# Kernel tuning notes

Hardware: AMD Instinct MI355X
Metric: run time of the kernel (lower is better)

Reference implementation:

```python
import jax, jax.numpy as jnp
import numpy as np

B, S, D, H = 4, 1024, 1024, 16
HD = D // H  # head_dim = 64


def setup_inputs() -> dict:
    key = jax.random.key(0)
    ks = jax.random.split(key, 16)
    w = lambda k: jax.random.normal(k, (D, D), dtype=jnp.float32) * 0.02
    b = lambda k: jax.random.normal(k, (D,), dtype=jnp.float32) * 0.02
    x = jax.random.normal(ks[0], (B, S, D), dtype=jnp.float32)
    mask = jnp.tril(jnp.ones((S, S), dtype=jnp.int32))[None, None]  # causal [1,1,S,S]
    bar_indices = jax.random.randint(ks[1], (S,), 0, S, dtype=jnp.int64)
    beat_indices = jax.random.randint(ks[2], (S,), 0, S, dtype=jnp.int64)
    return {
        "x": x, "mask": mask, "bar_indices": bar_indices, "beat_indices": beat_indices,
        "Wq": w(ks[3]), "bq": b(ks[4]), "Wk": w(ks[5]), "bk": b(ks[6]),
        "Wv": w(ks[7]), "bv": b(ks[8]),
        "W_bark": w(ks[9]), "b_bark": b(ks[10]),
        "W_beatk": w(ks[11]), "b_beatk": b(ks[12]),
        "Wo": w(ks[13]), "bo": b(ks[14]),
    }


def reference(x, mask, bar_indices, beat_indices, Wq, bq, Wk, bk, Wv, bv,
              W_bark, b_bark, W_beatk, b_beatk, Wo, bo):
    Bs, Sl, Dm = x.shape
    heads, hd = H, Dm // H

    def proj(t, W, b):  # torch Linear: t @ W.T + b, then split heads -> [B,H,S,hd]
        y = t @ W.T + b
        return y.reshape(Bs, -1, heads, hd).transpose(0, 2, 1, 3)

    q = proj(x, Wq, bq)
    k = proj(x, Wk, bk)
    v = proj(x, Wv, bv)
    scale = 1.0 / jnp.sqrt(jnp.asarray(hd, x.dtype))

    scores = jnp.einsum('bhqd,bhkd->bhqk', q, k) * scale

    # hierarchical bar bias (bar_query is computed but unused in the original)
    bar_k = proj(x[:, bar_indices], W_bark, b_bark)
    scores = scores + 0.2 * (jnp.einsum('bhqd,bhkd->bhqk', q, bar_k) * scale)

    # hierarchical beat bias
    beat_k = proj(x[:, beat_indices], W_beatk, b_beatk)
    scores = scores + 0.1 * (jnp.einsum('bhqd,bhkd->bhqk', q, beat_k) * scale)

    scores = jnp.where(mask == 0, jnp.asarray(-1e9, scores.dtype), scores)
    attn = jax.nn.softmax(scores, axis=-1)  # dropout is identity in eval

    out = jnp.einsum('bhqk,bhkd->bhqd', attn, v)
    out = out.transpose(0, 2, 1, 3).reshape(Bs, Sl, Dm)
    return out @ Wo.T + bo
```

## Files before the change

kernel.cpp:

```cpp
#include <hip/hip_runtime.h>
#include <hip/hip_bf16.h>


typedef __bf16 bf16x8 __attribute__((ext_vector_type(8)));
typedef __bf16 bf16x4 __attribute__((ext_vector_type(4)));
typedef float  f32x4  __attribute__((ext_vector_type(4)));

#define DMODEL 1024

#define ASYNC_LOAD16(gp, lp)                                                  \
    __builtin_amdgcn_global_load_lds(                                         \
        (const __attribute__((address_space(1))) unsigned int*)(gp),          \
        (__attribute__((address_space(3))) unsigned int*)(lp), 16, 0, 0)

__global__ __launch_bounds__(256) void cvt_kernel(
    const float* __restrict__ x,
    const float* __restrict__ Wq, const float* __restrict__ Wk,
    const float* __restrict__ Wv, const float* __restrict__ Wbar,
    const float* __restrict__ Wbeat, const float* __restrict__ Wo,
    __bf16* __restrict__ dst)
{
    const int g = blockIdx.x * 256 + threadIdx.x;
    const size_t e = (size_t)g * 8;
    const int seg = (int)(e >> 20);
    const float* src; size_t off; float s = 1.0f;
    if (seg < 4)       { src = x;     off = e; }
    else if (seg == 4) { src = Wq;    off = e - ((size_t)4 << 20); }
    else if (seg == 5) { src = Wk;    off = e - ((size_t)5 << 20); }
    else if (seg == 6) { src = Wv;    off = e - ((size_t)6 << 20); }
    else if (seg == 7) { src = Wbar;  off = e - ((size_t)7 << 20); s = 0.2f; }
    else if (seg == 8) { src = Wbeat; off = e - ((size_t)8 << 20); s = 0.1f; }
    else               { src = Wo;    off = e - ((size_t)9 << 20); }
    const float4 a = *(const float4*)&src[off];
    const float4 b = *(const float4*)&src[off + 4];
    bf16x8 v;
    v[0] = (__bf16)(a.x * s); v[1] = (__bf16)(a.y * s);
    v[2] = (__bf16)(a.z * s); v[3] = (__bf16)(a.w * s);
    v[4] = (__bf16)(b.x * s); v[5] = (__bf16)(b.y * s);
    v[6] = (__bf16)(b.z * s); v[7] = (__bf16)(b.w * s);
    *(bf16x8*)&dst[e] = v;
}


#define SWZ_COL(r_, ks_) \
    (((((ks_) * 64) + quad * 16) ^ (((r_) & 7) << 4)) >> 1)

#define READ_ALL(c_)                                                          \
    do {                                                                      \
        _Pragma("unroll") for (int mh = 0; mh < 2; ++mh)                      \
        _Pragma("unroll") for (int mi = 0; mi < 2; ++mi) {                    \
            const int r_ = ((w >> 2) << 5) + mh * 64 + mi * 16 + l15;         \
            _Pragma("unroll") for (int ks = 0; ks < 2; ++ks)                  \
                af[mh][mi][ks] = *(const bf16x8*)&Alds[(c_) * 8192 +          \
                                        r_ * 64 + SWZ_COL(r_, ks)];           \
        }                                                                     \
        _Pragma("unroll") for (int nh = 0; nh < 2; ++nh)                      \
        _Pragma("unroll") for (int nj = 0; nj < 2; ++nj) {                    \
            const int r_ = ((w & 3) << 5) + nh * 128 + nj * 16 + l15;         \
            _Pragma("unroll") for (int ks = 0; ks < 2; ++ks)                  \
                bfr[nh][nj][ks] = *(const bf16x8*)&Blds[(c_) * 16384 +        \
                                        r_ * 64 + SWZ_COL(r_, ks)];           \
        }                                                                     \
    } while (0)

#define STAGE_A1(bufn_, h_, kt_)                                              \
    do {                                                                      \
        const int tm_ = (kt_) >> 4;                                           \
        const int k0_ = ((kt_) & 15) << 6;                                    \
        const __bf16* ap_ = (tm_ == 0) ? aA0##h_ : (tm_ == 1) ? aA1##h_       \
                                                              : aA2##h_;      \
        ASYNC_LOAD16(ap_ + k0_,                                               \
                     &Alds[(bufn_) * 8192 + (h_) * 4096 + w * 512]);          \
    } while (0)

#define STAGE_B2(bufn_, h_, kt_)                                              \
    do {                                                                      \
        const int tm_ = (kt_) >> 4;                                           \
        const int k0_ = ((kt_) & 15) << 6;                                    \
        const __bf16* wp_ = (tm_ == 0) ? W0 : (tm_ == 1) ? W1 : W2;           \
        ASYNC_LOAD16(wp_ + bro##h_##0 + k0_,                                  \
                     &Blds[(bufn_) * 16384 + (h_) * 8192 + w * 512]);         \
        ASYNC_LOAD16(wp_ + bro##h_##1 + k0_,                                  \
                     &Blds[(bufn_) * 16384 + (h_) * 8192 + 4096 + w * 512]);  \
    } while (0)

#define PHASE_BAR1()                                                          \
    do {                                                                      \
        __builtin_amdgcn_s_barrier();                                         \
        asm volatile("s_waitcnt lgkmcnt(0)" ::: "memory");                    \
    } while (0)

#define MFMA16(nh_)                                                           \
    do {                                                                      \
        __builtin_amdgcn_s_setprio(1);                                        \
        _Pragma("unroll") for (int mh = 0; mh < 2; ++mh)                      \
        _Pragma("unroll") for (int mi = 0; mi < 2; ++mi)                      \
        _Pragma("unroll") for (int nj = 0; nj < 2; ++nj)                      \
        _Pragma("unroll") for (int ks = 0; ks < 2; ++ks) {                    \
            acc[mh * 2 + mi][(nh_) * 2 + nj] =                                \
                __builtin_amdgcn_mfma_f32_16x16x32_bf16(                      \
                    af[mh][mi][ks], bfr[(nh_)][nj][ks],                       \
                    acc[mh * 2 + mi][(nh_) * 2 + nj], 0, 0, 0);               \
        }                                                                     \
        __builtin_amdgcn_s_setprio(0);                                        \
    } while (0)

__global__ __launch_bounds__(512, 2) void gemm8p_kernel(
    const __bf16* __restrict__ xb,
    const __bf16* __restrict__ Wqb, const __bf16* __restrict__ Wkb,
    const __bf16* __restrict__ Wvb, const __bf16* __restrict__ Wbarb,
    const __bf16* __restrict__ Wbeatb,
    const float* __restrict__ bq, const float* __restrict__ bk,
    const float* __restrict__ bv, const float* __restrict__ bbar,
    const float* __restrict__ bbeat,
    const int* __restrict__ bar_idx, const int* __restrict__ beat_idx,
    __bf16* __restrict__ qbuf, __bf16* __restrict__ keffbuf,
    __bf16* __restrict__ vtbuf)
{
    __shared__ __align__(16) __bf16 Alds[3 * 8192];
    __shared__ __align__(16) __bf16 Blds[3 * 16384];

    const int bid = blockIdx.x;
    int mode, tk;
    if (bid < 128)      { mode = 1; tk = bid; }
    else if (bid < 256) { mode = 0; tk = bid - 128; }
    else                { mode = 2; tk = bid - 256; }
    const int m0 = (tk >> 2) << 7;
    const int n0 = (tk & 3) << 8;
    const int nkt = (mode == 1) ? 48 : 16;

    const int t    = (int)threadIdx.x;
    const int w    = t >> 6;
    const int lane = t & 63;
    const int l15  = lane & 15;
    const int quad = lane >> 4;

    const int srow = t >> 3;
    const int scol = ((((t & 7) * 16) ^ (((t >> 3) & 7) << 4)) >> 1);

    const __bf16* aA00 = xb + (size_t)(m0 + srow) * DMODEL + scol;
    const __bf16* aA01 = xb + (size_t)(m0 + 64 + srow) * DMODEL + scol;
    const __bf16* aA10 = aA00; const __bf16* aA11 = aA01;
    const __bf16* aA20 = aA00; const __bf16* aA21 = aA01;
    const __bf16 *W0, *W1, *W2;
    if (mode == 0)      { W0 = W1 = W2 = Wqb; }
    else if (mode == 2) { W0 = W1 = W2 = Wvb; }
    else {
        W0 = Wkb; W1 = Wbarb; W2 = Wbeatb;
        const int bb = m0 & ~1023;
        const int lr = m0 & 1023;
        aA10 = xb + (size_t)(bb + bar_idx[lr + srow]) * DMODEL + scol;
        aA11 = xb + (size_t)(bb + bar_idx[lr + 64 + srow]) * DMODEL + scol;
        aA20 = xb + (size_t)(bb + beat_idx[lr + srow]) * DMODEL + scol;
        aA21 = xb + (size_t)(bb + beat_idx[lr + 64 + srow]) * DMODEL + scol;
    }
    const size_t bro00 = (size_t)(n0 + srow) * DMODEL + scol;
    const size_t bro01 = (size_t)(n0 + 64 + srow) * DMODEL + scol;
    const size_t bro10 = (size_t)(n0 + 128 + srow) * DMODEL + scol;
    const size_t bro11 = (size_t)(n0 + 192 + srow) * DMODEL + scol;

    f32x4 acc[4][4];
#pragma unroll
    for (int i = 0; i < 4; ++i)
#pragma unroll
        for (int j = 0; j < 4; ++j)
            acc[i][j] = {0.f, 0.f, 0.f, 0.f};
    bf16x8 af[2][2][2], bfr[2][2][2];

    STAGE_A1(0, 0, 0);
    STAGE_A1(0, 1, 0);
    STAGE_B2(0, 0, 0);
    STAGE_B2(0, 1, 0);
    asm volatile("" ::: "memory");
    STAGE_A1(1, 0, 1);
    STAGE_A1(1, 1, 1);
    STAGE_B2(1, 0, 1);
    STAGE_B2(1, 1, 1);
    asm volatile("s_waitcnt vmcnt(6)" ::: "memory");
    __builtin_amdgcn_s_barrier();

    int rc = 0, fc = 2;
#pragma unroll 1
    for (int kt = 0; kt < nkt; ++kt) {
        const int kn = kt + 2;
        const bool st = (kn < nkt);

        READ_ALL(rc);
        if (st) { STAGE_A1(fc, 0, kn); STAGE_A1(fc, 1, kn); }
        PHASE_BAR1();
        MFMA16(0);

        if (st) { STAGE_B2(fc, 0, kn); STAGE_B2(fc, 1, kn); }
        if (kt < nkt - 2)
            asm volatile("s_waitcnt vmcnt(6)" ::: "memory");
        else if (kt == nkt - 2)
            asm volatile("s_waitcnt vmcnt(0)" ::: "memory");
        PHASE_BAR1();
        MFMA16(1);

        rc = (rc == 2) ? 0 : rc + 1;
        fc = (fc == 2) ? 0 : fc + 1;
    }

#pragma unroll
    for (int an = 0; an < 4; ++an) {
        const int col = n0 + ((w & 3) << 5) + (an >> 1) * 128 +
                        (an & 1) * 16 + l15;
        float bias;
        if (mode == 0)      bias = bq[col];
        else if (mode == 1) bias = bk[col] + 0.2f * bbar[col] + 0.1f * bbeat[col];
        else                bias = bv[col];
#pragma unroll
        for (int am = 0; am < 4; ++am) {
            const int rowbase = m0 + ((w >> 2) << 5) + (am >> 1) * 64 +
                                (am & 1) * 16 + quad * 4;
            if (mode == 2) {
                const int bb = rowbase >> 10;
                const int sb = rowbase & 1023;
                bf16x4 vv;
#pragma unroll
                for (int r = 0; r < 4; ++r) vv[r] = (__bf16)(acc[am][an][r] + bias);
                *(bf16x4*)&vtbuf[((size_t)(bb * 1024 + col)) * 1024 + sb] = vv;
            } else if (mode == 0) {
#pragma unroll
                for (int r = 0; r < 4; ++r)
                    qbuf[(size_t)(rowbase + r) * DMODEL + col] =
                        (__bf16)((acc[am][an][r] + bias) * 0.125f);
            } else {
#pragma unroll
                for (int r = 0; r < 4; ++r)
                    keffbuf[(size_t)(rowbase + r) * DMODEL + col] =
                        (__bf16)(acc[am][an][r] + bias);
            }
        }
    }
}

__global__ __launch_bounds__(256) void oproj_kernel(
    const __bf16* __restrict__ attnb, const __bf16* __restrict__ Wob,
    const float* __restrict__ bo, float* __restrict__ outb)
{
    const int tile = blockIdx.x;
    const int m0 = (tile >> 3) << 6;
    const int n0 = (tile & 7) << 7;

    __shared__ __align__(16) __bf16 Alds[64 * 32];
    __shared__ __align__(16) __bf16 Blds[128 * 32];

    const int t    = threadIdx.x;
    const int w    = t >> 6;
    const int lane = t & 63;
    const int l15  = lane & 15;
    const int quad = lane >> 4;
    const int wm   = (w >> 1) << 5;
    const int wn   = (w & 1) << 6;
    const int srow = t >> 2;
    const int scol = ((((t & 3) * 16) ^ (((t >> 2) & 3) << 4)) >> 1);
    const int rcol = (((quad * 16) ^ ((l15 & 3) << 4)) >> 1);

    const __bf16* gA  = attnb + (size_t)(m0 + srow) * DMODEL + scol;
    const __bf16* gB0 = Wob + (size_t)(n0 + srow) * DMODEL + scol;
    const __bf16* gB1 = Wob + (size_t)(n0 + 64 + srow) * DMODEL + scol;
    __bf16* lA  = &Alds[w * 512];
    __bf16* lB0 = &Blds[w * 512];
    __bf16* lB1 = &Blds[2048 + w * 512];

    f32x4 acc[2][4];
    for (int i = 0; i < 2; ++i)
        for (int j = 0; j < 4; ++j)
            acc[i][j] = {0.f, 0.f, 0.f, 0.f};

    for (int kk = 0; kk < 32; ++kk) {
        const int k0 = kk * 32;
        ASYNC_LOAD16(gA + k0, lA);
        ASYNC_LOAD16(gB0 + k0, lB0);
        ASYNC_LOAD16(gB1 + k0, lB1);
        __syncthreads();

        bf16x8 af[2], bfr[4];
        for (int i = 0; i < 2; ++i)
            af[i] = *(const bf16x8*)&Alds[(wm + i * 16 + l15) * 32 + rcol];
        for (int j = 0; j < 4; ++j)
            bfr[j] = *(const bf16x8*)&Blds[(wn + j * 16 + l15) * 32 + rcol];

        for (int i = 0; i < 2; ++i)
            for (int j = 0; j < 4; ++j)
                acc[i][j] = __builtin_amdgcn_mfma_f32_16x16x32_bf16(
                    af[i], bfr[j], acc[i][j], 0, 0, 0);
        __syncthreads();
    }

    for (int j = 0; j < 4; ++j) {
        const int col = n0 + wn + j * 16 + l15;
        const float bias = bo[col];
        for (int i = 0; i < 2; ++i) {
            const int rowbase = m0 + wm + i * 16 + quad * 4;
            for (int r = 0; r < 4; ++r)
                outb[(size_t)(rowbase + r) * DMODEL + col] = acc[i][j][r] + bias;
        }
    }
}

#define ATT_SLOT(q_, r_) ((((q_) ^ ((r_) & 7))) * 8)

__global__ __launch_bounds__(512) void attn_kernel(
    const __bf16* __restrict__ qbuf, const __bf16* __restrict__ keffbuf,
    const __bf16* __restrict__ vtbuf, __bf16* __restrict__ attnbuf)
{
    const int id = blockIdx.x;
    const int bh = id & 63;
    const int b  = bh >> 4;
    const int h  = bh & 15;
    const int qr = id >> 6;
    const int qt = (qr < 4) ? qr : 11 - qr;
    const int q0 = qt << 7;
    const int NT = 2 * qt + 2;

    __shared__ __align__(16) __bf16 Klds[2][64 * 64];
    __shared__ __align__(16) __bf16 Vlds[2][64 * 64];
    __shared__ __align__(16) __bf16 Plds[8][16][72];

    const int t    = (int)threadIdx.x;
    const int w    = t >> 6;
    const int lane = t & 63;
    const int l15  = lane & 15;
    const int quad = lane >> 4;

    const int srow = t >> 3;
    const int scol = ((t & 7) ^ (srow & 7)) * 8;

    const __bf16* gK = keffbuf + (size_t)(b * 1024 + srow) * DMODEL +
                       h * 64 + scol;
    const __bf16* gV = vtbuf + (size_t)(b * 1024 + h * 64 + srow) * 1024 +
                       scol;

    const __bf16* qbase =
        qbuf + (size_t)(b * 1024 + q0 + w * 16 + l15) * DMODEL + h * 64;
    bf16x8 qf0 = *(const bf16x8*)&qbase[quad * 8];
    bf16x8 qf1 = *(const bf16x8*)&qbase[32 + quad * 8];

    bf16x8 ones;
#pragma unroll
    for (int i = 0; i < 8; ++i) ones[i] = (__bf16)1.0f;

    f32x4 o[4];
#pragma unroll
    for (int i = 0; i < 4; ++i) o[i] = {0.f, 0.f, 0.f, 0.f};
    f32x4 lacc = {0.f, 0.f, 0.f, 0.f};

    ASYNC_LOAD16(gK, &Klds[0][t * 8]);
    ASYNC_LOAD16(gV, &Vlds[0][t * 8]);
    asm volatile("" ::: "memory");
    ASYNC_LOAD16(gK + (size_t)64 * DMODEL, &Klds[1][t * 8]);
    ASYNC_LOAD16(gV + 64, &Vlds[1][t * 8]);
    asm volatile("s_waitcnt vmcnt(2)" ::: "memory");
    __builtin_amdgcn_s_barrier();

#pragma unroll 1
    for (int j = 0; j < NT; ++j) {
        const int cur = j & 1;

        f32x4 sc[4];
#pragma unroll
        for (int nt = 0; nt < 4; ++nt) {
            const int row = nt * 16 + l15;
            bf16x8 kf0 = *(const bf16x8*)&Klds[cur][row * 64 +
                                                    ATT_SLOT(quad, row)];
            bf16x8 kf1 = *(const bf16x8*)&Klds[cur][row * 64 +
                                                    ATT_SLOT(quad + 4, row)];
            sc[nt] = {0.f, 0.f, 0.f, 0.f};
            sc[nt] = __builtin_amdgcn_mfma_f32_16x16x32_bf16(qf0, kf0, sc[nt], 0, 0, 0);
            sc[nt] = __builtin_amdgcn_mfma_f32_16x16x32_bf16(qf1, kf1, sc[nt], 0, 0, 0);
        }

        if (j >= NT - 2) {
            const int qrow_base = q0 + w * 16 + quad * 4;
#pragma unroll
            for (int nt = 0; nt < 4; ++nt) {
                const int kcol = j * 64 + nt * 16 + l15;
#pragma unroll
                for (int r = 0; r < 4; ++r)
                    if (kcol > qrow_base + r) sc[nt][r] = -1e30f;
            }
        }

#pragma unroll
        for (int nt = 0; nt < 4; ++nt)
#pragma unroll
            for (int r = 0; r < 4; ++r)
                sc[nt][r] = __expf(sc[nt][r]);

#pragma unroll
        for (int nt = 0; nt < 4; ++nt)
#pragma unroll
            for (int r = 0; r < 4; ++r)
                Plds[w][quad * 4 + r][nt * 16 + l15] = (__bf16)sc[nt][r];
        asm volatile("s_waitcnt lgkmcnt(0)" ::: "memory");

        bf16x8 pf0 = *(const bf16x8*)&Plds[w][l15][quad * 8];
        bf16x8 pf1 = *(const bf16x8*)&Plds[w][l15][32 + quad * 8];

        lacc = __builtin_amdgcn_mfma_f32_16x16x32_bf16(pf0, ones, lacc, 0, 0, 0);
        lacc = __builtin_amdgcn_mfma_f32_16x16x32_bf16(pf1, ones, lacc, 0, 0, 0);

#pragma unroll
        for (int nd = 0; nd < 4; ++nd) {
            const int row = nd * 16 + l15;
            bf16x8 vf0 = *(const bf16x8*)&Vlds[cur][row * 64 +
                                                    ATT_SLOT(quad, row)];
            bf16x8 vf1 = *(const bf16x8*)&Vlds[cur][row * 64 +
                                                    ATT_SLOT(quad + 4, row)];
            o[nd] = __builtin_amdgcn_mfma_f32_16x16x32_bf16(pf0, vf0, o[nd], 0, 0, 0);
            o[nd] = __builtin_amdgcn_mfma_f32_16x16x32_bf16(pf1, vf1, o[nd], 0, 0, 0);
        }

        __syncthreads();
        if (j + 2 < NT) {
            ASYNC_LOAD16(gK + (size_t)(j + 2) * 64 * DMODEL, &Klds[cur][t * 8]);
            ASYNC_LOAD16(gV + (size_t)(j + 2) * 64, &Vlds[cur][t * 8]);
        }
        if (j + 1 < NT) {
            if (j + 2 < NT)
                asm volatile("s_waitcnt vmcnt(2)" ::: "memory");
            else
                asm volatile("s_waitcnt vmcnt(0)" ::: "memory");
            __builtin_amdgcn_s_barrier();
        }
    }

    float rinv[4];
#pragma unroll
    for (int r = 0; r < 4; ++r) rinv[r] = 1.0f / lacc[r];
#pragma unroll
    for (int nd = 0; nd < 4; ++nd) {
#pragma unroll
        for (int r = 0; r < 4; ++r) {
            const int row = q0 + w * 16 + quad * 4 + r;
            attnbuf[(size_t)(b * 1024 + row) * DMODEL + h * 64 + nd * 16 + l15] =
                (__bf16)(o[nd][r] * rinv[r]);
        }
    }
}

extern "C" void kernel_launch(void* const* d_in, const int* in_sizes, int n_in,
                              void* d_out, int out_size, void* d_ws, size_t ws_size,
                              hipStream_t stream) {
    const float* x     = (const float*)d_in[0];
    const int* bar     = (const int*)d_in[2];
    const int* beat    = (const int*)d_in[3];
    const float* Wq    = (const float*)d_in[4];
    const float* bq    = (const float*)d_in[5];
    const float* Wk    = (const float*)d_in[6];
    const float* bk    = (const float*)d_in[7];
    const float* Wv    = (const float*)d_in[8];
    const float* bv    = (const float*)d_in[9];
    const float* Wbar  = (const float*)d_in[10];
    const float* bbar  = (const float*)d_in[11];
    const float* Wbeat = (const float*)d_in[12];
    const float* bbeat = (const float*)d_in[13];
    const float* Wo    = (const float*)d_in[14];
    const float* bo    = (const float*)d_in[15];

    const size_t M1 = (size_t)1 << 20;
    __bf16* xb     = (__bf16*)d_ws;
    __bf16* Wqb    = xb + 4 * M1;
    __bf16* Wkb    = Wqb + M1;
    __bf16* Wvb    = Wkb + M1;
    __bf16* Wbarb  = Wvb + M1;
    __bf16* Wbeatb = Wbarb + M1;
    __bf16* Wob    = Wbeatb + M1;
    __bf16* qbuf   = Wob + M1;
    __bf16* keff   = qbuf + 4 * M1;
    __bf16* vt     = keff + 4 * M1;
    __bf16* attn   = vt + 4 * M1;
    float*  outb   = (float*)d_out;

    cvt_kernel<<<5120, 256, 0, stream>>>(x, Wq, Wk, Wv, Wbar, Wbeat, Wo, xb);

    gemm8p_kernel<<<384, 512, 0, stream>>>(
        xb, Wqb, Wkb, Wvb, Wbarb, Wbeatb,
        bq, bk, bv, bbar, bbeat, bar, beat,
        qbuf, keff, vt);

    attn_kernel<<<512, 512, 0, stream>>>(qbuf, keff, vt, attn);

    oproj_kernel<<<512, 256, 0, stream>>>(attn, Wob, bo, outb);
}
```

Baseline: 205.5 us.

## Double-buffer LDS fragment registers and deepen async prefetch in projection GEMM

Restructures the projection GEMM main loop so the LDS reads for the next k-tile go into a second register set while the current set feeds the MFMAs. It also prefetches three tiles ahead instead of two and uses one barrier per k-tile instead of two. The goal is to hide LDS latency behind matrix math and cut synchronisation. In exchange it doubles the fragment registers, which at 512 threads with two blocks per CU risks spills or lower occupancy. The loop also steps two tiles at a time, which assumes an even tile count.

```diff
diff --git a/kernel.cpp b/kernel.cpp
--- a/kernel.cpp
+++ b/kernel.cpp
@@ -45,20 +45,20 @@
 #define SWZ_COL(r_, ks_) \
     (((((ks_) * 64) + quad * 16) ^ (((r_) & 7) << 4)) >> 1)
 
-#define READ_ALL(c_)                                                          \
+#define READ_SET(c_, AF_, BF_)                                                \
     do {                                                                      \
         _Pragma("unroll") for (int mh = 0; mh < 2; ++mh)                      \
         _Pragma("unroll") for (int mi = 0; mi < 2; ++mi) {                    \
             const int r_ = ((w >> 2) << 5) + mh * 64 + mi * 16 + l15;         \
             _Pragma("unroll") for (int ks = 0; ks < 2; ++ks)                  \
-                af[mh][mi][ks] = *(const bf16x8*)&Alds[(c_) * 8192 +          \
+                AF_[mh][mi][ks] = *(const bf16x8*)&Alds[(c_) * 8192 +         \
                                         r_ * 64 + SWZ_COL(r_, ks)];           \
         }                                                                     \
         _Pragma("unroll") for (int nh = 0; nh < 2; ++nh)                      \
         _Pragma("unroll") for (int nj = 0; nj < 2; ++nj) {                    \
             const int r_ = ((w & 3) << 5) + nh * 128 + nj * 16 + l15;         \
             _Pragma("unroll") for (int ks = 0; ks < 2; ++ks)                  \
-                bfr[nh][nj][ks] = *(const bf16x8*)&Blds[(c_) * 16384 +        \
+                BF_[nh][nj][ks] = *(const bf16x8*)&Blds[(c_) * 16384 +        \
                                         r_ * 64 + SWZ_COL(r_, ks)];           \
         }                                                                     \
     } while (0)
@@ -84,24 +84,24 @@
                      &Blds[(bufn_) * 16384 + (h_) * 8192 + 4096 + w * 512]);  \
     } while (0)
 
-#define PHASE_BAR1()                                                          \
+#define STAGE_TILE(bufn_, kt_)                                                \
     do {                                                                      \
-        __builtin_amdgcn_s_barrier();                                         \
-        asm volatile("s_waitcnt lgkmcnt(0)" ::: "memory");                    \
+        STAGE_A1(bufn_, 0, kt_); STAGE_A1(bufn_, 1, kt_);                     \
+        STAGE_B2(bufn_, 0, kt_); STAGE_B2(bufn_, 1, kt_);                     \
     } while (0)
 
-#define MFMA16(nh_)                                                           \
+#define MFMA32_SET(AF_, BF_)                                                  \
     do {                                                                      \
         __builtin_amdgcn_s_setprio(1);                                        \
+        _Pragma("unroll") for (int nh = 0; nh < 2; ++nh)                      \
         _Pragma("unroll") for (int mh = 0; mh < 2; ++mh)                      \
         _Pragma("unroll") for (int mi = 0; mi < 2; ++mi)                      \
         _Pragma("unroll") for (int nj = 0; nj < 2; ++nj)                      \
-        _Pragma("unroll") for (int ks = 0; ks < 2; ++ks) {                    \
-            acc[mh * 2 + mi][(nh_) * 2 + nj] =                                \
+        _Pragma("unroll") for (int ks = 0; ks < 2; ++ks)                      \
+            acc[mh * 2 + mi][nh * 2 + nj] =                                   \
                 __builtin_amdgcn_mfma_f32_16x16x32_bf16(                      \
-                    af[mh][mi][ks], bfr[(nh_)][nj][ks],                       \
-                    acc[mh * 2 + mi][(nh_) * 2 + nj], 0, 0, 0);               \
-        }                                                                     \
+                    AF_[mh][mi][ks], BF_[nh][nj][ks],                         \
+                    acc[mh * 2 + mi][nh * 2 + nj], 0, 0, 0);                  \
         __builtin_amdgcn_s_setprio(0);                                        \
     } while (0)
 
@@ -165,41 +165,42 @@
 #pragma unroll
         for (int j = 0; j < 4; ++j)
             acc[i][j] = {0.f, 0.f, 0.f, 0.f};
-    bf16x8 af[2][2][2], bfr[2][2][2];
-
-    STAGE_A1(0, 0, 0);
-    STAGE_A1(0, 1, 0);
-    STAGE_B2(0, 0, 0);
-    STAGE_B2(0, 1, 0);
+    bf16x8 afA[2][2][2], bfA[2][2][2];
+    bf16x8 afB[2][2][2], bfB[2][2][2];
+
+    STAGE_TILE(0, 0);
     asm volatile("" ::: "memory");
-    STAGE_A1(1, 0, 1);
-    STAGE_A1(1, 1, 1);
-    STAGE_B2(1, 0, 1);
-    STAGE_B2(1, 1, 1);
-    asm volatile("s_waitcnt vmcnt(6)" ::: "memory");
+    STAGE_TILE(1, 1);
+    asm volatile("" ::: "memory");
+    STAGE_TILE(2, 2);
+    asm volatile("s_waitcnt vmcnt(12)" ::: "memory");
     __builtin_amdgcn_s_barrier();
-
-    int rc = 0, fc = 2;
+    READ_SET(0, afA, bfA);
+
+    int sb = 0, rb = 1;
 #pragma unroll 1
-    for (int kt = 0; kt < nkt; ++kt) {
-        const int kn = kt + 2;
-        const bool st = (kn < nkt);
-
-        READ_ALL(rc);
-        if (st) { STAGE_A1(fc, 0, kn); STAGE_A1(fc, 1, kn); }
-        PHASE_BAR1();
-        MFMA16(0);
-
-        if (st) { STAGE_B2(fc, 0, kn); STAGE_B2(fc, 1, kn); }
-        if (kt < nkt - 2)
-            asm volatile("s_waitcnt vmcnt(6)" ::: "memory");
-        else if (kt == nkt - 2)
-            asm volatile("s_waitcnt vmcnt(0)" ::: "memory");
-        PHASE_BAR1();
-        MFMA16(1);
-
-        rc = (rc == 2) ? 0 : rc + 1;
-        fc = (fc == 2) ? 0 : fc + 1;
+    for (int kt = 0; kt < nkt; kt += 2) {
+        if (kt + 2 < nkt)
+            asm volatile("s_waitcnt vmcnt(6) lgkmcnt(0)" ::: "memory");
+        else
+            asm volatile("s_waitcnt vmcnt(0) lgkmcnt(0)" ::: "memory");
+        __builtin_amdgcn_s_barrier();
+        if (kt + 3 < nkt) STAGE_TILE(sb, kt + 3);
+        READ_SET(rb, afB, bfB);
+        MFMA32_SET(afA, bfA);
+        sb = (sb == 2) ? 0 : sb + 1;
+        rb = (rb == 2) ? 0 : rb + 1;
+
+        if (kt + 3 < nkt)
+            asm volatile("s_waitcnt vmcnt(6) lgkmcnt(0)" ::: "memory");
+        else
+            asm volatile("s_waitcnt vmcnt(0) lgkmcnt(0)" ::: "memory");
+        __builtin_amdgcn_s_barrier();
+        if (kt + 4 < nkt) STAGE_TILE(sb, kt + 4);
+        if (kt + 2 < nkt) READ_SET(rb, afA, bfA);
+        MFMA32_SET(afB, bfB);
+        sb = (sb == 2) ? 0 : sb + 1;
+        rb = (rb == 2) ? 0 : rb + 1;
     }
 
 #pragma unroll
@@ -216,11 +217,11 @@
                                 (am & 1) * 16 + quad * 4;
             if (mode == 2) {
                 const int bb = rowbase >> 10;
-                const int sb = rowbase & 1023;
+                const int sb2 = rowbase & 1023;
                 bf16x4 vv;
 #pragma unroll
                 for (int r = 0; r < 4; ++r) vv[r] = (__bf16)(acc[am][an][r] + bias);
-                *(bf16x4*)&vtbuf[((size_t)(bb * 1024 + col)) * 1024 + sb] = vv;
+                *(bf16x4*)&vtbuf[((size_t)(bb * 1024 + col)) * 1024 + sb2] = vv;
             } else if (mode == 0) {
 #pragma unroll
                 for (int r = 0; r < 4; ++r)
```

Measured after the change: 219.3 us. 6.7% more time.
